# Optimization experiments

Measured on AMD Instinct MI355X. Metric: run time of the kernel, lower is better.

## Reference

```python
import jax, jax.numpy as jnp
import numpy as np

GRADIENT_SCALE = 1.0  # undefined global in the source; standard surrogate scale
ALPHA = 0.9
BETA = 0.8
THRESHOLD = 1.0
FEATURES = 512
UNITS = 1024
TIME = 256
BATCH = 128

@jax.custom_vjp
def heaviside(x):
    return jnp.where(x > 0, jnp.ones_like(x), jnp.zeros_like(x))

def _heaviside_fwd(x):
    return heaviside(x), x

def _heaviside_bwd(x, dy):
    # dy * GRADIENT_SCALE * (1/(|x|+1))^2  (surrogate gradient from tf.custom_gradient)
    return (dy * (GRADIENT_SCALE * jnp.square(1.0 / (jnp.abs(x) + 1.0))),)

heaviside.defvjp(_heaviside_fwd, _heaviside_bwd)


def setup_inputs() -> dict:
    key = jax.random.key(0)
    k1, k2 = jax.random.split(key)
    inputs = jax.random.normal(k1, (BATCH, FEATURES, TIME), dtype=jnp.float32)
    # keras add_weight default initializer ~ glorot_uniform; any float init is fine for a numerics baseline
    limit = np.sqrt(6.0 / (FEATURES + UNITS)).astype(np.float32)
    w = jax.random.uniform(k2, (FEATURES, UNITS), dtype=jnp.float32, minval=-limit, maxval=limit)
    return {"inputs": inputs, "w": w}


def reference(inputs, w):
    # In the original tf.while_loop body, membrane_potential, synapse and prev_s are
    # returned UNMODIFIED, so they remain zero for every timestep. The recurrence
    # therefore collapses exactly to, per step t:
    #   h_t = x[:, :, t] @ w
    #   i_t = alpha*0 + h_t = h_t
    #   v_t = (beta*0 + h_t) * (threshold - 0) = h_t * threshold
    #   s_t = heaviside(v_t - threshold)
    # which is timestep-independent and can be computed as one batched GEMM.
    h = jnp.einsum('bft,fu->btu', inputs, w)        # [B, T, U]
    v = (BETA * 0.0 + h) * (THRESHOLD - 0.0)        # state terms are identically zero
    s = heaviside(v - THRESHOLD)                    # [B, T, U]
    return jnp.transpose(s, (0, 2, 1))              # [B, U, T], matching tf transpose perm=[1,2,0]
```

## Files before the change

kernel.cpp:

```cpp
#include <hip/hip_runtime.h>


#define BB 128
#define FF 512
#define TT 256
#define UU 1024

__global__ __launch_bounds__(256, 4)
void snn_gemm_kernel(const float* __restrict__ in, const float* __restrict__ w,
                     float* __restrict__ out) {
    __shared__ float As[16][128];
    __shared__ float Bs[16][128];

    const int b  = blockIdx.z;
    const int u0 = blockIdx.y * 128;
    const int t0 = blockIdx.x * 128;

    const float* __restrict__ inb  = in  + (size_t)b * FF * TT;
    float* __restrict__       outb = out + (size_t)b * UU * TT;

    const int tid = threadIdx.x;
    const int tx  = tid & 15;
    const int ty  = tid >> 4;

    const int k0 = tid >> 5;
    const int c0 = (tid & 31) * 4;
    const int k1 = k0 + 8;

    float acc[8][8];
#pragma unroll
    for (int i = 0; i < 8; i++)
#pragma unroll
        for (int j = 0; j < 8; j++) acc[i][j] = 0.0f;

    float4 a_r0 = *(const float4*)&w[(size_t)k0 * UU + u0 + c0];
    float4 a_r1 = *(const float4*)&w[(size_t)k1 * UU + u0 + c0];
    float4 b_r0 = *(const float4*)&inb[k0 * TT + t0 + c0];
    float4 b_r1 = *(const float4*)&inb[k1 * TT + t0 + c0];

    for (int f0 = 0; f0 < FF; f0 += 16) {
        *(float4*)&As[k0][c0] = a_r0;
        *(float4*)&As[k1][c0] = a_r1;
        *(float4*)&Bs[k0][c0] = b_r0;
        *(float4*)&Bs[k1][c0] = b_r1;
        __syncthreads();

        if (f0 + 16 < FF) {
            const int fn = f0 + 16;
            a_r0 = *(const float4*)&w[(size_t)(fn + k0) * UU + u0 + c0];
            a_r1 = *(const float4*)&w[(size_t)(fn + k1) * UU + u0 + c0];
            b_r0 = *(const float4*)&inb[(fn + k0) * TT + t0 + c0];
            b_r1 = *(const float4*)&inb[(fn + k1) * TT + t0 + c0];
        }

#pragma unroll
        for (int k = 0; k < 16; k++) {
            const float4 a0 = *(const float4*)&As[k][ty * 4];
            const float4 a1 = *(const float4*)&As[k][ty * 4 + 64];
            const float4 v0 = *(const float4*)&Bs[k][tx * 4];
            const float4 v1 = *(const float4*)&Bs[k][tx * 4 + 64];
            const float am[8] = {a0.x, a0.y, a0.z, a0.w, a1.x, a1.y, a1.z, a1.w};
            const float bn[8] = {v0.x, v0.y, v0.z, v0.w, v1.x, v1.y, v1.z, v1.w};
#pragma unroll
            for (int i = 0; i < 8; i++)
#pragma unroll
                for (int j = 0; j < 8; j++)
                    acc[i][j] = fmaf(am[i], bn[j], acc[i][j]);
        }
        __syncthreads();
    }

#pragma unroll
    for (int i = 0; i < 8; i++) {
        const int m = (i < 4) ? (ty * 4 + i) : (64 + ty * 4 + i - 4);
        float* __restrict__ orow = outb + (size_t)(u0 + m) * TT + t0;
        float4 o0, o1;
        o0.x = acc[i][0] > 1.0f ? 1.0f : 0.0f;
        o0.y = acc[i][1] > 1.0f ? 1.0f : 0.0f;
        o0.z = acc[i][2] > 1.0f ? 1.0f : 0.0f;
        o0.w = acc[i][3] > 1.0f ? 1.0f : 0.0f;
        o1.x = acc[i][4] > 1.0f ? 1.0f : 0.0f;
        o1.y = acc[i][5] > 1.0f ? 1.0f : 0.0f;
        o1.z = acc[i][6] > 1.0f ? 1.0f : 0.0f;
        o1.w = acc[i][7] > 1.0f ? 1.0f : 0.0f;
        *(float4*)&orow[tx * 4]      = o0;
        *(float4*)&orow[tx * 4 + 64] = o1;
    }
}

extern "C" void kernel_launch(void* const* d_in, const int* in_sizes, int n_in,
                              void* d_out, int out_size, void* d_ws, size_t ws_size,
                              hipStream_t stream) {
    const float* in = (const float*)d_in[0];
    const float* w  = (const float*)d_in[1];
    float* out      = (float*)d_out;

    dim3 grid(TT / 128, UU / 128, BB);
    snn_gemm_kernel<<<grid, dim3(256), 0, stream>>>(in, w, out);
}
```

Baseline: 550.1 us.

## Restructure GEMM to one wavefront per block with broadcast weights and async LDS loads

Replaces the 256-thread 128x128 tiled kernel with a single-wave kernel where each lane computes 4 time columns for 32 units across the full time range. Weights are read directly from global memory as uniform vector loads, and input rows are staged into a double-buffered LDS tile using direct global-to-LDS loads. This is meant to cut LDS traffic and barrier cost, at the price of more global/L2 weight traffic, fewer threads per block, and reliance on correct ordering of asynchronous LDS loads.

```diff
diff --git a/kernel.cpp b/kernel.cpp
--- a/kernel.cpp
+++ b/kernel.cpp
@@ -1,90 +1,89 @@
 #include <hip/hip_runtime.h>
 
 
-#define BB 128
 #define FF 512
 #define TT 256
 #define UU 1024
+#define BK 8
+#define MW 32
 
-__global__ __launch_bounds__(256, 4)
-void snn_gemm_kernel(const float* __restrict__ in, const float* __restrict__ w,
-                     float* __restrict__ out) {
-    __shared__ float As[16][128];
-    __shared__ float Bs[16][128];
+typedef float floatx16 __attribute__((ext_vector_type(16)));
 
-    const int b  = blockIdx.z;
-    const int u0 = blockIdx.y * 128;
-    const int t0 = blockIdx.x * 128;
+__global__ __launch_bounds__(64, 3)
+void snn_wave_gemm(const float* __restrict__ in, const float* __restrict__ w,
+                   float* __restrict__ out) {
+    __shared__ float Bs[2][BK][TT];
 
-    const float* __restrict__ inb  = in  + (size_t)b * FF * TT;
-    float* __restrict__       outb = out + (size_t)b * UU * TT;
+    const int b    = blockIdx.y;
+    const int u0   = blockIdx.x * MW;
+    const int lane = threadIdx.x;
 
-    const int tid = threadIdx.x;
-    const int tx  = tid & 15;
-    const int ty  = tid >> 4;
+    const float* __restrict__ inb = in + (size_t)b * FF * TT;
 
-    const int k0 = tid >> 5;
-    const int c0 = (tid & 31) * 4;
-    const int k1 = k0 + 8;
+    float4 acc[MW];
+#pragma unroll
+    for (int i = 0; i < MW; i++) acc[i] = float4{0.f, 0.f, 0.f, 0.f};
 
-    float acc[8][8];
 #pragma unroll
-    for (int i = 0; i < 8; i++)
-#pragma unroll
-        for (int j = 0; j < 8; j++) acc[i][j] = 0.0f;
+    for (int r = 0; r < BK; r++) {
+        __builtin_amdgcn_global_load_lds(
+            (const __attribute__((address_space(1))) void*)(inb + r * TT + lane * 4),
+            (__attribute__((address_space(3))) void*)&Bs[0][r][0],
+            16, 0, 0);
+    }
 
-    float4 a_r0 = *(const float4*)&w[(size_t)k0 * UU + u0 + c0];
-    float4 a_r1 = *(const float4*)&w[(size_t)k1 * UU + u0 + c0];
-    float4 b_r0 = *(const float4*)&inb[k0 * TT + t0 + c0];
-    float4 b_r1 = *(const float4*)&inb[k1 * TT + t0 + c0];
+    for (int f0 = 0; f0 < FF; f0 += BK) {
+        const int buf = (f0 / BK) & 1;
 
-    for (int f0 = 0; f0 < FF; f0 += 16) {
-        *(float4*)&As[k0][c0] = a_r0;
-        *(float4*)&As[k1][c0] = a_r1;
-        *(float4*)&Bs[k0][c0] = b_r0;
-        *(float4*)&Bs[k1][c0] = b_r1;
         __syncthreads();
 
-        if (f0 + 16 < FF) {
-            const int fn = f0 + 16;
-            a_r0 = *(const float4*)&w[(size_t)(fn + k0) * UU + u0 + c0];
-            a_r1 = *(const float4*)&w[(size_t)(fn + k1) * UU + u0 + c0];
-            b_r0 = *(const float4*)&inb[(fn + k0) * TT + t0 + c0];
-            b_r1 = *(const float4*)&inb[(fn + k1) * TT + t0 + c0];
+        if (f0 + BK < FF) {
+#pragma unroll
+            for (int r = 0; r < BK; r++) {
+                __builtin_amdgcn_global_load_lds(
+                    (const __attribute__((address_space(1))) void*)
+                        (inb + (f0 + BK + r) * TT + lane * 4),
+                    (__attribute__((address_space(3))) void*)&Bs[buf ^ 1][r][0],
+                    16, 0, 0);
+            }
         }
 
 #pragma unroll
-        for (int k = 0; k < 16; k++) {
-            const float4 a0 = *(const float4*)&As[k][ty * 4];
-            const float4 a1 = *(const float4*)&As[k][ty * 4 + 64];
-            const float4 v0 = *(const float4*)&Bs[k][tx * 4];
-            const float4 v1 = *(const float4*)&Bs[k][tx * 4 + 64];
-            const float am[8] = {a0.x, a0.y, a0.z, a0.w, a1.x, a1.y, a1.z, a1.w};
-            const float bn[8] = {v0.x, v0.y, v0.z, v0.w, v1.x, v1.y, v1.z, v1.w};
+        for (int k = 0; k < BK; k++) {
+            const int f = f0 + k;
+            const floatx16* __restrict__ pa =
+                (const floatx16*)(w + (size_t)f * UU + u0);
+            const floatx16 aL = pa[0];
+            const floatx16 aH = pa[1];
+
+            const float4 vb = *(const float4*)&Bs[buf][k][lane * 4];
+
 #pragma unroll
-            for (int i = 0; i < 8; i++)
+            for (int i = 0; i < 16; i++) {
+                acc[i].x = fmaf(aL[i], vb.x, acc[i].x);
+                acc[i].y = fmaf(aL[i], vb.y, acc[i].y);
+                acc[i].z = fmaf(aL[i], vb.z, acc[i].z);
+                acc[i].w = fmaf(aL[i], vb.w, acc[i].w);
+            }
 #pragma unroll
-                for (int j = 0; j < 8; j++)
-                    acc[i][j] = fmaf(am[i], bn[j], acc[i][j]);
+            for (int i = 0; i < 16; i++) {
+                acc[16 + i].x = fmaf(aH[i], vb.x, acc[16 + i].x);
+                acc[16 + i].y = fmaf(aH[i], vb.y, acc[16 + i].y);
+                acc[16 + i].z = fmaf(aH[i], vb.z, acc[16 + i].z);
+                acc[16 + i].w = fmaf(aH[i], vb.w, acc[16 + i].w);
+            }
         }
-        __syncthreads();
     }
 
+    float* __restrict__ outb = out + ((size_t)b * UU + u0) * TT;
 #pragma unroll
-    for (int i = 0; i < 8; i++) {
-        const int m = (i < 4) ? (ty * 4 + i) : (64 + ty * 4 + i - 4);
-        float* __restrict__ orow = outb + (size_t)(u0 + m) * TT + t0;
-        float4 o0, o1;
-        o0.x = acc[i][0] > 1.0f ? 1.0f : 0.0f;
-        o0.y = acc[i][1] > 1.0f ? 1.0f : 0.0f;
-        o0.z = acc[i][2] > 1.0f ? 1.0f : 0.0f;
-        o0.w = acc[i][3] > 1.0f ? 1.0f : 0.0f;
-        o1.x = acc[i][4] > 1.0f ? 1.0f : 0.0f;
-        o1.y = acc[i][5] > 1.0f ? 1.0f : 0.0f;
-        o1.z = acc[i][6] > 1.0f ? 1.0f : 0.0f;
-        o1.w = acc[i][7] > 1.0f ? 1.0f : 0.0f;
-        *(float4*)&orow[tx * 4]      = o0;
-        *(float4*)&orow[tx * 4 + 64] = o1;
+    for (int i = 0; i < MW; i++) {
+        float4 o;
+        o.x = acc[i].x > 1.0f ? 1.0f : 0.0f;
+        o.y = acc[i].y > 1.0f ? 1.0f : 0.0f;
+        o.z = acc[i].z > 1.0f ? 1.0f : 0.0f;
+        o.w = acc[i].w > 1.0f ? 1.0f : 0.0f;
+        *(float4*)&outb[(size_t)i * TT + lane * 4] = o;
     }
 }
 
@@ -95,6 +94,6 @@
     const float* w  = (const float*)d_in[1];
     float* out      = (float*)d_out;
 
-    dim3 grid(TT / 128, UU / 128, BB);
-    snn_gemm_kernel<<<grid, dim3(256), 0, stream>>>(in, w, out);
+    dim3 grid(UU / MW, 128);
+    snn_wave_gemm<<<grid, dim3(64), 0, stream>>>(in, w, out);
 }
```

Measured after the change: 1.085 ms. 97.3% more time.
